# Performance work log

Measured on AMD Instinct MI355X. Metric: run time of the kernel, lower is better.

The kernel has to match this reference:

```python
import jax, jax.numpy as jnp
import numpy as np

N_NODES = 50000
N_EDGES = 600000
D = 128
HIDDEN = 128
OUT = 1


def setup_inputs() -> dict:
    key = jax.random.key(0)
    ks = jax.random.split(key, 6)
    z = jax.random.normal(ks[0], (N_NODES, D), dtype=jnp.float32)
    e = jax.random.randint(ks[1], (2, N_EDGES), 0, N_NODES, dtype=jnp.int64)
    # Linear weights in [in, out] layout; scaled like torch default init
    W1 = jax.random.normal(ks[2], (2 * D, HIDDEN), dtype=jnp.float32) / np.sqrt(2 * D)
    b1 = jax.random.normal(ks[3], (HIDDEN,), dtype=jnp.float32) / np.sqrt(2 * D)
    W2 = jax.random.normal(ks[4], (HIDDEN, OUT), dtype=jnp.float32) / np.sqrt(HIDDEN)
    b2 = jax.random.normal(ks[5], (OUT,), dtype=jnp.float32) / np.sqrt(HIDDEN)
    return {"z": z, "e": e, "W1": W1, "b1": b1, "W2": W2, "b2": b2}


def reference(z, e, W1, b1, W2, b2):
    x_i = z[e[0]]                      # [E, D] gather source nodes
    x_j = z[e[1]]                      # [E, D] gather target nodes
    x = jnp.concatenate([x_i, x_j], axis=1)  # [E, 2D]
    h = jax.nn.relu(x @ W1 + b1)       # [E, HIDDEN]
    out = h @ W2 + b2                  # [E, OUT]
    return jax.nn.sigmoid(out).squeeze()  # [E]
```

## Files before the change

### kernel.cpp

```cpp
#include <hip/hip_runtime.h>


#define DD 128

typedef __attribute__((ext_vector_type(8))) short short8;
typedef __attribute__((ext_vector_type(4))) float floatx4;

static __device__ __forceinline__ unsigned short f2bf(float f) {
  unsigned int u = __builtin_bit_cast(unsigned int, f);
  u += 0x7fffu + ((u >> 16) & 1u);
  return (unsigned short)(u >> 16);
}

__global__ __launch_bounds__(256) void wt_build(
    const float* __restrict__ W1, unsigned short* __restrict__ Wt) {
  const int g = blockIdx.x * 256 + threadIdx.x;
  const int c = g >> 5;
  const int kq = (g & 31) * 4;
  const float* src = (c < 128) ? (W1 + c) : (W1 + 128 * 128 + (c - 128));
  ushort4 o;
  o.x = f2bf(src[(size_t)(kq + 0) * 128]);
  o.y = f2bf(src[(size_t)(kq + 1) * 128]);
  o.z = f2bf(src[(size_t)(kq + 2) * 128]);
  o.w = f2bf(src[(size_t)(kq + 3) * 128]);
  *(ushort4*)&Wt[c * 128 + kq] = o;
}

__global__ __launch_bounds__(512, 4) void node_mfma(
    const float* __restrict__ z, const unsigned short* __restrict__ Wt,
    const float* __restrict__ b1, signed char* __restrict__ gqi,
    signed char* __restrict__ gqj, float* __restrict__ sci,
    float* __restrict__ scj, int n_nodes) {
  __shared__ __align__(16) unsigned short zb[64 * 136];
  __shared__ unsigned int ep[2 * 64 * 33];
  __shared__ unsigned int smax[2][64];
  const int tid = threadIdx.x;
  const int nb = blockIdx.x * 64;

  if (tid < 128) smax[tid >> 6][tid & 63] = 0u;

#pragma unroll
  for (int i = 0; i < 4; ++i) {
    int q = tid + i * 512;
    int nl = q >> 5;
    int node = nb + nl; if (node >= n_nodes) node = n_nodes - 1;
    float4 v = ((const float4*)z)[(size_t)node * 32 + (q & 31)];
    ushort4 o;
    o.x = f2bf(v.x); o.y = f2bf(v.y); o.z = f2bf(v.z); o.w = f2bf(v.w);
    *(ushort4*)&zb[nl * 136 + (q & 31) * 4] = o;
  }

  const int w = tid >> 6, lane = tid & 63;
  const int l15 = lane & 15, quad = lane >> 4;

  short8 a[2][4];
#pragma unroll
  for (int tt = 0; tt < 2; ++tt) {
    const unsigned short* wrow =
        Wt + (size_t)((w * 2 + tt) * 16 + l15) * 128 + quad * 8;
#pragma unroll
    for (int s = 0; s < 4; ++s) a[tt][s] = *(const short8*)(wrow + s * 32);
  }

  floatx4 acc[2][4];
#pragma unroll
  for (int tt = 0; tt < 2; ++tt) {
    floatx4 bias = {0.f, 0.f, 0.f, 0.f};
    if (w < 4) {
      float4 b4 = *(const float4*)&b1[(w * 2 + tt) * 16 + quad * 4];
      bias[0] = b4.x; bias[1] = b4.y; bias[2] = b4.z; bias[3] = b4.w;
    }
#pragma unroll
    for (int nt = 0; nt < 4; ++nt) acc[tt][nt] = bias;
  }

  __syncthreads();

#pragma unroll
  for (int nt = 0; nt < 4; ++nt) {
    short8 bz[4];
#pragma unroll
    for (int s = 0; s < 4; ++s)
      bz[s] = *(const short8*)&zb[(nt * 16 + l15) * 136 + s * 32 + quad * 8];
#pragma unroll
    for (int tt = 0; tt < 2; ++tt)
#pragma unroll
      for (int s = 0; s < 4; ++s)
        acc[tt][nt] = __builtin_amdgcn_mfma_f32_16x16x32_bf16(
            a[tt][s], bz[s], acc[tt][nt], 0, 0, 0);
  }

  const int half = w >> 2;
  const int cbase = (w & 3) * 32;

#pragma unroll
  for (int nt = 0; nt < 4; ++nt) {
    float m = 0.f;
#pragma unroll
    for (int tt = 0; tt < 2; ++tt)
#pragma unroll
      for (int r = 0; r < 4; ++r) m = fmaxf(m, fabsf(acc[tt][nt][r]));
    m = fmaxf(m, __shfl_xor(m, 16));
    m = fmaxf(m, __shfl_xor(m, 32));
    if (lane < 16)
      atomicMax(&smax[half][nt * 16 + lane], __float_as_uint(m));
  }
  __syncthreads();

#pragma unroll
  for (int nt = 0; nt < 4; ++nt) {
    const int node_l = nt * 16 + l15;
    const float am = __uint_as_float(smax[half][node_l]);
    const float inv = (am > 0.f) ? 127.f / am : 0.f;
#pragma unroll
    for (int tt = 0; tt < 2; ++tt) {
      unsigned int v = 0;
#pragma unroll
      for (int r = 0; r < 4; ++r) {
        const int q = (int)rintf(acc[tt][nt][r] * inv);
        v |= ((unsigned int)(q & 0xff)) << (8 * r);
      }
      ep[half * 2112 + node_l * 33 + ((cbase + tt * 16 + quad * 4) >> 2)] = v;
    }
  }
  __syncthreads();

  {
    const int hh = tid >> 8;
    const int sub = tid & 255;
    const int nl = sub >> 2;
    const int c32 = (sub & 3) * 32;
    const int node = nb + nl;
    const unsigned int* rp = &ep[hh * 2112 + nl * 33 + (c32 >> 2)];
    uint4 o0, o1;
    o0.x = rp[0]; o0.y = rp[1]; o0.z = rp[2]; o0.w = rp[3];
    o1.x = rp[4]; o1.y = rp[5]; o1.z = rp[6]; o1.w = rp[7];
    if (node < n_nodes) {
      signed char* dq = hh ? gqj : gqi;
      uint4* gp = (uint4*)(dq + (size_t)node * 128 + c32);
      gp[0] = o0; gp[1] = o1;
    }
    if (tid < 128) {
      const int h2 = tid >> 6, n2 = tid & 63;
      const int node2 = nb + n2;
      if (node2 < n_nodes) {
        const float amv = __uint_as_float(smax[h2][n2]);
        (h2 ? scj : sci)[node2] = amv * (1.f / 127.f);
      }
    }
  }
}

__global__ __launch_bounds__(256) void edge_mlp_q(
    const int* __restrict__ e, const signed char* __restrict__ gqi,
    const signed char* __restrict__ gqj, const float* __restrict__ sci,
    const float* __restrict__ scj, const float* __restrict__ W2,
    const float* __restrict__ b2, float* __restrict__ out, int E) {
  const int p = threadIdx.x & 7;
  const float4* wv = (const float4*)W2;
  float4 W[4];
#pragma unroll
  for (int k = 0; k < 4; ++k) W[k] = wv[p * 4 + k];
  const float bias2 = b2[0];

  const int stride = gridDim.x * 32;
  for (int edge = blockIdx.x * 32 + (threadIdx.x >> 3); edge < E; edge += stride) {
    const int i = e[edge];
    const int j = e[E + edge];
    const float si = sci[i];
    const float sj = scj[j];
    const uint4 qa = ((const uint4*)(gqi + (size_t)i * 128))[p];
    const uint4 qb = ((const uint4*)(gqj + (size_t)j * 128))[p];
    const unsigned int ua[4] = {qa.x, qa.y, qa.z, qa.w};
    const unsigned int ub[4] = {qb.x, qb.y, qb.z, qb.w};
    float acc = 0.f;
#pragma unroll
    for (int k = 0; k < 4; ++k) {
      const float wk[4] = {W[k].x, W[k].y, W[k].z, W[k].w};
#pragma unroll
      for (int b = 0; b < 4; ++b) {
        const float af = (float)(int)(signed char)(ua[k] >> (8 * b));
        const float bf = (float)(int)(signed char)(ub[k] >> (8 * b));
        const float h = fmaf(si, af, sj * bf);
        acc = fmaf(fmaxf(h, 0.f), wk[b], acc);
      }
    }
    acc += __shfl_xor(acc, 1);
    acc += __shfl_xor(acc, 2);
    acc += __shfl_xor(acc, 4);
    if (p == 0) {
      out[edge] = 1.f / (1.f + __expf(-(acc + bias2)));
    }
  }
}

__global__ __launch_bounds__(256) void edge_direct(
    const int* __restrict__ e, const float* __restrict__ z,
    const float* __restrict__ W1, const float* __restrict__ b1,
    const float* __restrict__ W2, const float* __restrict__ b2,
    float* __restrict__ out, int E) {
  const int lane = threadIdx.x & 63;
  const int edge = (int)((blockIdx.x * 256u + threadIdx.x) >> 6);
  if (edge >= E) return;
  const int i = e[edge], j = e[E + edge];
  const float* zi = z + (size_t)i * 128;
  const float* zj = z + (size_t)j * 128;
  const int c0 = lane * 2;
  float h0 = b1[c0], h1 = b1[c0 + 1];
  for (int k = 0; k < 128; ++k) {
    float a = zi[k], b = zj[k];
    float2 wt = *(const float2*)&W1[(size_t)k * 128 + c0];
    float2 wb = *(const float2*)&W1[(size_t)(128 + k) * 128 + c0];
    h0 = fmaf(a, wt.x, h0); h1 = fmaf(a, wt.y, h1);
    h0 = fmaf(b, wb.x, h0); h1 = fmaf(b, wb.y, h1);
  }
  float s = fmaxf(h0, 0.f) * W2[c0] + fmaxf(h1, 0.f) * W2[c0 + 1];
#pragma unroll
  for (int off = 1; off < 64; off <<= 1) s += __shfl_xor(s, off);
  if (lane == 0) out[edge] = 1.f / (1.f + __expf(-(s + b2[0])));
}

extern "C" void kernel_launch(void* const* d_in, const int* in_sizes, int n_in,
                              void* d_out, int out_size, void* d_ws, size_t ws_size,
                              hipStream_t stream) {
  const float* z  = (const float*)d_in[0];
  const int*   e  = (const int*)d_in[1];
  const float* W1 = (const float*)d_in[2];
  const float* b1 = (const float*)d_in[3];
  const float* W2 = (const float*)d_in[4];
  const float* b2 = (const float*)d_in[5];
  float* out = (float*)d_out;
  const int n_nodes = in_sizes[0] / DD;
  const int E = in_sizes[1] / 2;

  const size_t gq_bytes = (size_t)n_nodes * DD;
  const size_t sc_bytes = (size_t)n_nodes * sizeof(float);
  const size_t wt_bytes = 256 * 128 * sizeof(unsigned short);
  const size_t need = 2 * gq_bytes + 2 * sc_bytes + wt_bytes;

  if (ws_size >= need && n_nodes > 0) {
    signed char* gqi = (signed char*)d_ws;
    signed char* gqj = gqi + gq_bytes;
    float* sci = (float*)((char*)d_ws + 2 * gq_bytes);
    float* scj = (float*)((char*)d_ws + 2 * gq_bytes + sc_bytes);
    unsigned short* Wt =
        (unsigned short*)((char*)d_ws + 2 * gq_bytes + 2 * sc_bytes);
    wt_build<<<32, 256, 0, stream>>>(W1, Wt);
    node_mfma<<<(n_nodes + 63) / 64, 512, 0, stream>>>(z, Wt, b1, gqi, gqj,
                                                       sci, scj, n_nodes);
    edge_mlp_q<<<2048, 256, 0, stream>>>(e, gqi, gqj, sci, scj, W2, b2, out, E);
  } else {
    edge_direct<<<(E + 3) / 4, 256, 0, stream>>>(e, z, W1, b1, W2, b2, out, E);
  }
}
```

Measured before the change: 113.9 us.

## Fuse weight prep, node MFMA and edge MLP into one cooperative kernel

Replaces the three separate launches (weight transpose, node projection with int8 quantization, edge gather MLP) with a single cooperative persistent kernel that uses grid-wide syncs between phases. The aim is to remove the launch gaps and tail effects between kernels. The grid is capped at 512 blocks and limited by an occupancy query, with a fallback to the old three-kernel path if the cooperative launch fails. In exchange it pays for two grid barriers, and the node phase now loops over tiles with fewer resident blocks, while the edge phase runs with a different grid and block shape than before.

```diff
diff --git a/kernel.cpp b/kernel.cpp
--- a/kernel.cpp
+++ b/kernel.cpp
@@ -1,4 +1,7 @@
 #include <hip/hip_runtime.h>
+#include <hip/hip_cooperative_groups.h>
+
+namespace cg = cooperative_groups;
 
 
 #define DD 128
@@ -10,6 +13,188 @@
   unsigned int u = __builtin_bit_cast(unsigned int, f);
   u += 0x7fffu + ((u >> 16) & 1u);
   return (unsigned short)(u >> 16);
+}
+
+__global__ __launch_bounds__(512, 4) void fused_all(
+    const float* __restrict__ z, const int* __restrict__ e,
+    const float* __restrict__ W1, const float* __restrict__ b1,
+    const float* __restrict__ W2, const float* __restrict__ b2,
+    float* __restrict__ out, signed char* __restrict__ gqi,
+    signed char* __restrict__ gqj, float* __restrict__ sci,
+    float* __restrict__ scj, unsigned short* __restrict__ Wt,
+    int n_nodes, int E) {
+  cg::grid_group grid = cg::this_grid();
+  __shared__ __align__(16) unsigned short zb[64 * 136];
+  __shared__ unsigned int ep[2 * 64 * 33];
+  __shared__ unsigned int smax[2][64];
+  const int tid = threadIdx.x;
+
+  if (blockIdx.x < 16) {
+    const int g = blockIdx.x * 512 + tid;
+    const int c = g >> 5;
+    const int kq = (g & 31) * 4;
+    const float* src = (c < 128) ? (W1 + c) : (W1 + 128 * 128 + (c - 128));
+    ushort4 o;
+    o.x = f2bf(src[(size_t)(kq + 0) * 128]);
+    o.y = f2bf(src[(size_t)(kq + 1) * 128]);
+    o.z = f2bf(src[(size_t)(kq + 2) * 128]);
+    o.w = f2bf(src[(size_t)(kq + 3) * 128]);
+    *(ushort4*)&Wt[c * 128 + kq] = o;
+  }
+  grid.sync();
+
+  const int w = tid >> 6, lane = tid & 63;
+  const int l15 = lane & 15, quad = lane >> 4;
+  const int ntiles = (n_nodes + 63) >> 6;
+
+  short8 a[2][4];
+#pragma unroll
+  for (int tt = 0; tt < 2; ++tt) {
+    const unsigned short* wrow =
+        Wt + (size_t)((w * 2 + tt) * 16 + l15) * 128 + quad * 8;
+#pragma unroll
+    for (int s = 0; s < 4; ++s) a[tt][s] = *(const short8*)(wrow + s * 32);
+  }
+  floatx4 biasv[2];
+#pragma unroll
+  for (int tt = 0; tt < 2; ++tt) {
+    floatx4 b = {0.f, 0.f, 0.f, 0.f};
+    if (w < 4) {
+      float4 b4 = *(const float4*)&b1[(w * 2 + tt) * 16 + quad * 4];
+      b[0] = b4.x; b[1] = b4.y; b[2] = b4.z; b[3] = b4.w;
+    }
+    biasv[tt] = b;
+  }
+  const int half = w >> 2;
+  const int cbase = (w & 3) * 32;
+
+  for (int tile = blockIdx.x; tile < ntiles; tile += gridDim.x) {
+    const int nb = tile * 64;
+    if (tid < 128) smax[tid >> 6][tid & 63] = 0u;
+#pragma unroll
+    for (int i = 0; i < 4; ++i) {
+      int q = tid + i * 512;
+      int nl = q >> 5;
+      int node = nb + nl; if (node >= n_nodes) node = n_nodes - 1;
+      float4 v = ((const float4*)z)[(size_t)node * 32 + (q & 31)];
+      ushort4 o;
+      o.x = f2bf(v.x); o.y = f2bf(v.y); o.z = f2bf(v.z); o.w = f2bf(v.w);
+      *(ushort4*)&zb[nl * 136 + (q & 31) * 4] = o;
+    }
+    floatx4 acc[2][4];
+#pragma unroll
+    for (int tt = 0; tt < 2; ++tt)
+#pragma unroll
+      for (int nt = 0; nt < 4; ++nt) acc[tt][nt] = biasv[tt];
+    __syncthreads();
+
+#pragma unroll
+    for (int nt = 0; nt < 4; ++nt) {
+      short8 bz[4];
+#pragma unroll
+      for (int s = 0; s < 4; ++s)
+        bz[s] = *(const short8*)&zb[(nt * 16 + l15) * 136 + s * 32 + quad * 8];
+#pragma unroll
+      for (int tt = 0; tt < 2; ++tt)
+#pragma unroll
+        for (int s = 0; s < 4; ++s)
+          acc[tt][nt] = __builtin_amdgcn_mfma_f32_16x16x32_bf16(
+              a[tt][s], bz[s], acc[tt][nt], 0, 0, 0);
+    }
+
+#pragma unroll
+    for (int nt = 0; nt < 4; ++nt) {
+      float m = 0.f;
+#pragma unroll
+      for (int tt = 0; tt < 2; ++tt)
+#pragma unroll
+        for (int r = 0; r < 4; ++r) m = fmaxf(m, fabsf(acc[tt][nt][r]));
+      m = fmaxf(m, __shfl_xor(m, 16));
+      m = fmaxf(m, __shfl_xor(m, 32));
+      if (lane < 16)
+        atomicMax(&smax[half][nt * 16 + lane], __float_as_uint(m));
+    }
+    __syncthreads();
+#pragma unroll
+    for (int nt = 0; nt < 4; ++nt) {
+      const int node_l = nt * 16 + l15;
+      const float am = __uint_as_float(smax[half][node_l]);
+      const float inv = (am > 0.f) ? 127.f / am : 0.f;
+#pragma unroll
+      for (int tt = 0; tt < 2; ++tt) {
+        unsigned int v = 0;
+#pragma unroll
+        for (int r = 0; r < 4; ++r) {
+          const int q = (int)rintf(acc[tt][nt][r] * inv);
+          v |= ((unsigned int)(q & 0xff)) << (8 * r);
+        }
+        ep[half * 2112 + node_l * 33 + ((cbase + tt * 16 + quad * 4) >> 2)] = v;
+      }
+    }
+    __syncthreads();
+    {
+      const int hh = tid >> 8;
+      const int sub = tid & 255;
+      const int nl = sub >> 2;
+      const int c32 = (sub & 3) * 32;
+      const int node = nb + nl;
+      const unsigned int* rp = &ep[hh * 2112 + nl * 33 + (c32 >> 2)];
+      uint4 o0, o1;
+      o0.x = rp[0]; o0.y = rp[1]; o0.z = rp[2]; o0.w = rp[3];
+      o1.x = rp[4]; o1.y = rp[5]; o1.z = rp[6]; o1.w = rp[7];
+      if (node < n_nodes) {
+        signed char* dq = hh ? gqj : gqi;
+        uint4* gp = (uint4*)(dq + (size_t)node * 128 + c32);
+        gp[0] = o0; gp[1] = o1;
+      }
+      if (tid < 128) {
+        const int h2 = tid >> 6, n2 = tid & 63;
+        const int node2 = nb + n2;
+        if (node2 < n_nodes) {
+          const float amv = __uint_as_float(smax[h2][n2]);
+          (h2 ? scj : sci)[node2] = amv * (1.f / 127.f);
+        }
+      }
+    }
+    __syncthreads();
+  }
+  grid.sync();
+
+  {
+    const int p = tid & 7;
+    const float4* wv = (const float4*)W2;
+    float4 W[4];
+#pragma unroll
+    for (int k = 0; k < 4; ++k) W[k] = wv[p * 4 + k];
+    const float bias2 = b2[0];
+    const int stride = gridDim.x * 64;
+    for (int edge = blockIdx.x * 64 + (tid >> 3); edge < E; edge += stride) {
+      const int i = e[edge];
+      const int j = e[E + edge];
+      const float si = sci[i];
+      const float sj = scj[j];
+      const uint4 qa = ((const uint4*)(gqi + (size_t)i * 128))[p];
+      const uint4 qb = ((const uint4*)(gqj + (size_t)j * 128))[p];
+      const unsigned int ua[4] = {qa.x, qa.y, qa.z, qa.w};
+      const unsigned int ub[4] = {qb.x, qb.y, qb.z, qb.w};
+      float acc = 0.f;
+#pragma unroll
+      for (int k = 0; k < 4; ++k) {
+        const float wk[4] = {W[k].x, W[k].y, W[k].z, W[k].w};
+#pragma unroll
+        for (int b = 0; b < 4; ++b) {
+          const float af = (float)(int)(signed char)(ua[k] >> (8 * b));
+          const float bf = (float)(int)(signed char)(ub[k] >> (8 * b));
+          const float h = fmaf(si, af, sj * bf);
+          acc = fmaf(fmaxf(h, 0.f), wk[b], acc);
+        }
+      }
+      acc += __shfl_xor(acc, 1);
+      acc += __shfl_xor(acc, 2);
+      acc += __shfl_xor(acc, 4);
+      if (p == 0) out[edge] = 1.f / (1.f + __expf(-(acc + bias2)));
+    }
+  }
 }
 
 __global__ __launch_bounds__(256) void wt_build(
@@ -38,7 +223,6 @@
   const int nb = blockIdx.x * 64;
 
   if (tid < 128) smax[tid >> 6][tid & 63] = 0u;
-
 #pragma unroll
   for (int i = 0; i < 4; ++i) {
     int q = tid + i * 512;
@@ -49,10 +233,8 @@
     o.x = f2bf(v.x); o.y = f2bf(v.y); o.z = f2bf(v.z); o.w = f2bf(v.w);
     *(ushort4*)&zb[nl * 136 + (q & 31) * 4] = o;
   }
-
   const int w = tid >> 6, lane = tid & 63;
   const int l15 = lane & 15, quad = lane >> 4;
-
   short8 a[2][4];
 #pragma unroll
   for (int tt = 0; tt < 2; ++tt) {
@@ -61,7 +243,6 @@
 #pragma unroll
     for (int s = 0; s < 4; ++s) a[tt][s] = *(const short8*)(wrow + s * 32);
   }
-
   floatx4 acc[2][4];
 #pragma unroll
   for (int tt = 0; tt < 2; ++tt) {
@@ -73,9 +254,7 @@
 #pragma unroll
     for (int nt = 0; nt < 4; ++nt) acc[tt][nt] = bias;
   }
-
   __syncthreads();
-
 #pragma unroll
   for (int nt = 0; nt < 4; ++nt) {
     short8 bz[4];
@@ -89,10 +268,8 @@
         acc[tt][nt] = __builtin_amdgcn_mfma_f32_16x16x32_bf16(
             a[tt][s], bz[s], acc[tt][nt], 0, 0, 0);
   }
-
   const int half = w >> 2;
   const int cbase = (w & 3) * 32;
-
 #pragma unroll
   for (int nt = 0; nt < 4; ++nt) {
     float m = 0.f;
@@ -106,7 +283,6 @@
       atomicMax(&smax[half][nt * 16 + lane], __float_as_uint(m));
   }
   __syncthreads();
-
 #pragma unroll
   for (int nt = 0; nt < 4; ++nt) {
     const int node_l = nt * 16 + l15;
@@ -124,7 +300,6 @@
     }
   }
   __syncthreads();
-
   {
     const int hh = tid >> 8;
     const int sub = tid & 255;
@@ -162,7 +337,6 @@
 #pragma unroll
   for (int k = 0; k < 4; ++k) W[k] = wv[p * 4 + k];
   const float bias2 = b2[0];
-
   const int stride = gridDim.x * 32;
   for (int edge = blockIdx.x * 32 + (threadIdx.x >> 3); edge < E; edge += stride) {
     const int i = e[edge];
@@ -188,9 +362,7 @@
     acc += __shfl_xor(acc, 1);
     acc += __shfl_xor(acc, 2);
     acc += __shfl_xor(acc, 4);
-    if (p == 0) {
-      out[edge] = 1.f / (1.f + __expf(-(acc + bias2)));
-    }
+    if (p == 0) out[edge] = 1.f / (1.f + __expf(-(acc + bias2)));
   }
 }
 
@@ -245,10 +417,38 @@
     float* scj = (float*)((char*)d_ws + 2 * gq_bytes + sc_bytes);
     unsigned short* Wt =
         (unsigned short*)((char*)d_ws + 2 * gq_bytes + 2 * sc_bytes);
-    wt_build<<<32, 256, 0, stream>>>(W1, Wt);
-    node_mfma<<<(n_nodes + 63) / 64, 512, 0, stream>>>(z, Wt, b1, gqi, gqj,
-                                                       sci, scj, n_nodes);
-    edge_mlp_q<<<2048, 256, 0, stream>>>(e, gqi, gqj, sci, scj, W2, b2, out, E);
+
+    int maxB = 0;
+    hipError_t oe = hipOccupancyMaxActiveBlocksPerMultiprocessor(
+        &maxB, (const void*)fused_all, 512, 0);
+    int grid = 512;
+    if (oe == hipSuccess && maxB > 0) {
+      int cap = maxB * 256;
+      if (grid > cap) grid = cap;
+    }
+    bool done = false;
+    if (oe == hipSuccess && grid >= 16) {
+      const float* z_ = z; const int* e_ = e;
+      const float* W1_ = W1; const float* b1_ = b1;
+      const float* W2_ = W2; const float* b2_ = b2;
+      float* out_ = out;
+      signed char* gqi_ = gqi; signed char* gqj_ = gqj;
+      float* sci_ = sci; float* scj_ = scj;
+      unsigned short* Wt_ = Wt;
+      int nn = n_nodes, EE = E;
+      void* args[] = {&z_, &e_, &W1_, &b1_, &W2_, &b2_, &out_,
+                      &gqi_, &gqj_, &sci_, &scj_, &Wt_, &nn, &EE};
+      hipError_t le = hipLaunchCooperativeKernel(
+          (const void*)fused_all, dim3(grid), dim3(512), args, 0, stream);
+      done = (le == hipSuccess);
+    }
+    if (!done) {
+      wt_build<<<32, 256, 0, stream>>>(W1, Wt);
+      node_mfma<<<(n_nodes + 63) / 64, 512, 0, stream>>>(z, Wt, b1, gqi, gqj,
+                                                         sci, scj, n_nodes);
+      edge_mlp_q<<<2048, 256, 0, stream>>>(e, gqi, gqj, sci, scj, W2, b2, out,
+                                           E);
+    }
   } else {
     edge_direct<<<(E + 3) / 4, 256, 0, stream>>>(e, z, W1, b1, W2, b2, out, E);
   }
```

Result: slower. 196.5 us (+72.5%).
